# Optimization experiments

Hardware: AMD Instinct MI355X
Metric: run time of the kernel (lower is better)

## Reference

```python
import jax, jax.numpy as jnp
import numpy as np

HIDDEN = 1024
B, S = 4, 2048

def setup_inputs() -> dict:
    key = jax.random.key(0)
    k1, k2 = jax.random.split(key)
    qkv = jax.random.normal(k1, (B, S, HIDDEN), dtype=jnp.float32)
    mask = jnp.ones((B, S), dtype=jnp.float32)
    W_qkv = jax.random.normal(k2, (HIDDEN, 3 * HIDDEN), dtype=jnp.float32) * (HIDDEN ** -0.5)
    b_qkv = jnp.zeros((3 * HIDDEN,), dtype=jnp.float32)
    return {"qkv": qkv, "mask": mask, "W_qkv": W_qkv, "b_qkv": b_qkv}

def reference(qkv, mask, W_qkv, b_qkv):
    scale = HIDDEN ** -0.5
    proj = jnp.einsum("bsi,ih->bsh", qkv, W_qkv) + b_qkv  # [B,S,3H]
    q, k, v = jnp.split(proj, 3, axis=-1)                  # each [B,S,H]
    q = q * scale
    scores = jnp.einsum("bqh,bkh->bqk", q, k)              # [B,S,S]
    scores = scores + (1.0 - mask)[:, None, :] * -10000.0
    dist = jax.nn.softmax(scores, axis=-1)                 # dropout = identity (eval)
    return jnp.einsum("bqk,bkh->bqh", dist, v)             # [B,S,H]
```

## Files before the change

### kernel.cpp

```cpp
#include <hip/hip_runtime.h>
#include <hip/hip_bf16.h>

#define HID   1024
#define H3    3072
#define SEQ   2048
#define NB    4
#define MTOT  8192

typedef __bf16 bf16;
typedef bf16  bf16x4 __attribute__((ext_vector_type(4)));
typedef bf16  bf16x8 __attribute__((ext_vector_type(8)));
typedef float f32x4  __attribute__((ext_vector_type(4)));

#define MFMA16(a, b, c) __builtin_amdgcn_mfma_f32_16x16x32_bf16((a), (b), (c), 0, 0, 0)

#define GLOAD_LDS16(gp, lp)                                                     \
    __builtin_amdgcn_global_load_lds(                                           \
        (const __attribute__((address_space(1))) void*)(gp),                    \
        (__attribute__((address_space(3))) void*)(lp), 16, 0, 0)

#define FENCE() asm volatile("" ::: "memory")

__device__ __forceinline__ void stage_half(
    const bf16* __restrict__ G, long ld, long row0, long col0,
    char* dstbase, int w, int lane)
{
    const int r  = lane >> 2;
    const int c0 = ((lane & 3) * 8) ^ (((lane >> 5) & 1) << 4);
#pragma unroll
    for (int l = 0; l < 2; ++l) {
        const int sh = l * 8 + w;
        const bf16* src = G + (row0 + (long)((sh >> 1) * 16 + r)) * ld
                            + col0 + ((sh & 1) * 32 + c0);
        GLOAD_LDS16(src, dstbase + sh * 1024);
    }
}

__device__ __forceinline__ void gemm256_core(
    const bf16* __restrict__ A, long lda,
    const bf16* __restrict__ Bt, long ldb,
    long m0, long n0, int NT, char* lds, f32x4 (&acc)[8][4])
{
    const int tid = threadIdx.x, lane = tid & 63, w = tid >> 6;
    const int lr = lane & 15, lkg = lane >> 4;
    const int subA = (w >> 2) * 8;
    const int subB = (w & 3) * 4;
    const int inner = lr * 64 + (((lkg * 8) ^ ((lr >> 3) << 4)) << 1);

    char* A0b = lds;
    char* B0b = lds + 32768;
    char* A1b = lds + 65536;
    char* B1b = lds + 98304;

    stage_half(A,  lda, m0,        0, A0b,          w, lane);
    stage_half(A,  lda, m0 + 128,  0, A0b + 16384,  w, lane);
    stage_half(Bt, ldb, n0,        0, B0b,          w, lane);
    stage_half(Bt, ldb, n0 + 128,  0, B0b + 16384,  w, lane);
    stage_half(Bt, ldb, n0,       64, B1b,          w, lane);
    stage_half(Bt, ldb, n0 + 128, 64, B1b + 16384,  w, lane);
    asm volatile("s_waitcnt vmcnt(0)" ::: "memory");
    __builtin_amdgcn_s_barrier();
    FENCE();

    bf16x8 aR[4][2], bR[4][2];

    for (int t = 0; t < NT; ++t) {
        char* Ac = (t & 1) ? A1b : A0b;
        char* Bc = (t & 1) ? B1b : B0b;
        char* An = (t & 1) ? A0b : A1b;
        const long kA = (long)(t + 1) * 64;
        const long kB = (long)(t + 2) * 64;
        const bool doA = (t + 1 < NT), doB = (t + 2 < NT);

#pragma unroll
        for (int mf = 0; mf < 4; ++mf)
#pragma unroll
            for (int ks = 0; ks < 2; ++ks)
                aR[mf][ks] = *(const bf16x8*)(Ac + ((subA + mf) * 2 + ks) * 1024 + inner);
#pragma unroll
        for (int nf = 0; nf < 2; ++nf)
#pragma unroll
            for (int ks = 0; ks < 2; ++ks)
                bR[nf][ks] = *(const bf16x8*)(Bc + ((subB + nf) * 2 + ks) * 1024 + inner);
        if (doA) stage_half(A, lda, m0, kA, An, w, lane);
        __builtin_amdgcn_s_barrier();
        __builtin_amdgcn_s_setprio(1);
#pragma unroll
        for (int mf = 0; mf < 4; ++mf)
#pragma unroll
            for (int nf = 0; nf < 2; ++nf)
#pragma unroll
                for (int ks = 0; ks < 2; ++ks)
                    acc[mf][nf] = MFMA16(aR[mf][ks], bR[nf][ks], acc[mf][nf]);
        __builtin_amdgcn_s_setprio(0);
        __builtin_amdgcn_s_barrier();
        FENCE();

#pragma unroll
        for (int nf = 0; nf < 2; ++nf)
#pragma unroll
            for (int ks = 0; ks < 2; ++ks)
                bR[2 + nf][ks] = *(const bf16x8*)(Bc + ((subB + 2 + nf) * 2 + ks) * 1024 + inner);
        if (doA) stage_half(A, lda, m0 + 128, kA, An + 16384, w, lane);
        __builtin_amdgcn_s_barrier();
        __builtin_amdgcn_s_setprio(1);
#pragma unroll
        for (int mf = 0; mf < 4; ++mf)
#pragma unroll
            for (int nf = 0; nf < 2; ++nf)
#pragma unroll
                for (int ks = 0; ks < 2; ++ks)
                    acc[mf][2 + nf] = MFMA16(aR[mf][ks], bR[2 + nf][ks], acc[mf][2 + nf]);
        __builtin_amdgcn_s_setprio(0);
        __builtin_amdgcn_s_barrier();
        FENCE();

#pragma unroll
        for (int mf = 0; mf < 4; ++mf)
#pragma unroll
            for (int ks = 0; ks < 2; ++ks)
                aR[mf][ks] = *(const bf16x8*)(Ac + ((subA + 4 + mf) * 2 + ks) * 1024 + inner);
        if (doB) stage_half(Bt, ldb, n0, kB, Bc, w, lane);
        __builtin_amdgcn_s_barrier();
        __builtin_amdgcn_s_setprio(1);
#pragma unroll
        for (int mf = 0; mf < 4; ++mf)
#pragma unroll
            for (int nf = 0; nf < 2; ++nf)
#pragma unroll
                for (int ks = 0; ks < 2; ++ks)
                    acc[4 + mf][nf] = MFMA16(aR[mf][ks], bR[nf][ks], acc[4 + mf][nf]);
        __builtin_amdgcn_s_setprio(0);
        __builtin_amdgcn_s_barrier();
        FENCE();

        if (doB) {
            stage_half(Bt, ldb, n0 + 128, kB, Bc + 16384, w, lane);
            asm volatile("s_waitcnt vmcnt(4)" ::: "memory");
        } else {
            asm volatile("s_waitcnt vmcnt(0)" ::: "memory");
        }
        __builtin_amdgcn_s_barrier();
        __builtin_amdgcn_s_setprio(1);
#pragma unroll
        for (int mf = 0; mf < 4; ++mf)
#pragma unroll
            for (int nf = 0; nf < 2; ++nf)
#pragma unroll
                for (int ks = 0; ks < 2; ++ks)
                    acc[4 + mf][2 + nf] = MFMA16(aR[mf][ks], bR[2 + nf][ks], acc[4 + mf][2 + nf]);
        __builtin_amdgcn_s_setprio(0);
        __builtin_amdgcn_s_barrier();
        FENCE();
    }
}

__global__ __launch_bounds__(256) void conv_kernel(
    const float* __restrict__ X, const float* __restrict__ W,
    bf16* __restrict__ Xb, bf16* __restrict__ Wt)
{
    __shared__ bf16 T[64][66];
    const int bid = blockIdx.x;
    if (bid < 4096) {
        const long i = ((long)bid * 256 + threadIdx.x) * 8;
        float4 a = *(const float4*)(X + i);
        float4 b = *(const float4*)(X + i + 4);
        bf16x8 o;
        o[0] = (bf16)a.x; o[1] = (bf16)a.y; o[2] = (bf16)a.z; o[3] = (bf16)a.w;
        o[4] = (bf16)b.x; o[5] = (bf16)b.y; o[6] = (bf16)b.z; o[7] = (bf16)b.w;
        *(bf16x8*)(Xb + i) = o;
    } else {
        const int b2 = bid - 4096;
        const int n0 = (b2 % 48) * 64, k0 = (b2 / 48) * 64;
        const int r = threadIdx.x >> 2, s = threadIdx.x & 3;
        const float* wp = W + (size_t)(k0 + r) * H3 + n0 + s * 16;
#pragma unroll
        for (int q = 0; q < 4; ++q) {
            float4 a = *(const float4*)(wp + q * 4);
            T[r][s * 16 + q * 4 + 0] = (bf16)a.x;
            T[r][s * 16 + q * 4 + 1] = (bf16)a.y;
            T[r][s * 16 + q * 4 + 2] = (bf16)a.z;
            T[r][s * 16 + q * 4 + 3] = (bf16)a.w;
        }
        __syncthreads();
        bf16x8 o0, o1;
#pragma unroll
        for (int i = 0; i < 8; ++i) o0[i] = T[s * 16 + i][r];
#pragma unroll
        for (int i = 0; i < 8; ++i) o1[i] = T[s * 16 + 8 + i][r];
        bf16* op = Wt + (size_t)(n0 + r) * HID + k0 + s * 16;
        *(bf16x8*)op       = o0;
        *(bf16x8*)(op + 8) = o1;
    }
}

__global__ __launch_bounds__(512, 2) void proj_gemm2(
    const bf16* __restrict__ Xb, const bf16* __restrict__ Wt,
    const float* __restrict__ bias,
    bf16* __restrict__ Qb, bf16* __restrict__ Kb, bf16* __restrict__ Vt)
{
    __shared__ __attribute__((aligned(16))) char lds[135168];
    const int x = blockIdx.x & 7, q = blockIdx.x >> 3;
    const int bn = q >> 2, bm = x * 4 + (q & 3);

    f32x4 acc[8][4] = {};
    gemm256_core(Xb, HID, Wt, HID, (long)bm * 256, (long)bn * 256, 16, lds, acc);

    const int tid = threadIdx.x, lane = tid & 63, w = tid >> 6;
    const int lr = lane & 15, lkg = lane >> 4;
    const int wmL = (w >> 2) * 128;
    const int wnL = (w & 3) * 64;
    const int seg = bn >> 2;

    __syncthreads();
    bf16* sm_ = (bf16*)lds;

    if (seg < 2) {
        const float qs = (seg == 0) ? 0.03125f : 1.0f;
#pragma unroll
        for (int nf = 0; nf < 4; ++nf) {
            const int nl = wnL + nf * 16 + lr;
            const float bv = bias[bn * 256 + nl];
#pragma unroll
            for (int mf = 0; mf < 8; ++mf) {
                const int ml = wmL + mf * 16 + lkg * 4;
#pragma unroll
                for (int j = 0; j < 4; ++j)
                    sm_[(ml + j) * 264 + nl] = (bf16)((acc[mf][nf][j] + bv) * qs);
            }
        }
        __syncthreads();
        bf16* dst = (seg == 0) ? Qb : Kb;
        const long colbase = (long)(bn & 3) * 256;
        const long rowbase = (long)bm * 256;
#pragma unroll
        for (int it = 0; it < 16; ++it) {
            const int ml = (tid >> 5) + it * 16;
            const int nc = (tid & 31) * 8;
            bf16x8 vv = *(const bf16x8*)&sm_[ml * 264 + nc];
            *(bf16x8*)&dst[(rowbase + ml) * HID + colbase + nc] = vv;
        }
    } else {
#pragma unroll
        for (int nf = 0; nf < 4; ++nf) {
            const int nl = wnL + nf * 16 + lr;
            const float bv = bias[bn * 256 + nl];
#pragma unroll
            for (int mf = 0; mf < 8; ++mf) {
                const int ml = wmL + mf * 16 + lkg * 4;
                bf16x4 pk;
#pragma unroll
                for (int j = 0; j < 4; ++j) pk[j] = (bf16)(acc[mf][nf][j] + bv);
                *(bf16x4*)&sm_[nl * 264 + ml] = pk;
            }
        }
        __syncthreads();
        const int  bb = bm >> 3;
        const long s0 = (long)(bm & 7) * 256;
        const long h0 = (long)bn * 256 - 2048;
#pragma unroll
        for (int it = 0; it < 16; ++it) {
            const int nl = (tid >> 5) + it * 16;
            const int mc = (tid & 31) * 8;
            bf16x8 vv = *(const bf16x8*)&sm_[nl * 264 + mc];
            *(bf16x8*)&Vt[((long)(bb << 10) + h0 + nl) * SEQ + s0 + mc] = vv;
        }
    }
}

__global__ __launch_bounds__(512, 2) void qk_gemm2(
    const bf16* __restrict__ Qb, const bf16* __restrict__ Kb,
    float* __restrict__ Sc, int b_base)
{
    __shared__ __attribute__((aligned(16))) char lds[131072];
    const int z = blockIdx.z, b = b_base + z;

    f32x4 acc[8][4] = {};
    gemm256_core(Qb + (size_t)b * SEQ * HID, HID,
                 Kb + (size_t)b * SEQ * HID, HID,
                 (long)blockIdx.x * 256, (long)blockIdx.y * 256, 16, lds, acc);

    const int tid = threadIdx.x, lane = tid & 63, w = tid >> 6;
    const int lr = lane & 15, lkg = lane >> 4;
    const int m0i = (int)blockIdx.x * 256 + (w >> 2) * 128;
    const int n0i = (int)blockIdx.y * 256 + (w & 3) * 64;
    float* C = Sc + (size_t)z * SEQ * SEQ;
#pragma unroll
    for (int mf = 0; mf < 8; ++mf)
#pragma unroll
        for (int j = 0; j < 4; ++j) {
            const int row = m0i + mf * 16 + lkg * 4 + j;
#pragma unroll
            for (int nf = 0; nf < 4; ++nf)
                C[(size_t)row * SEQ + n0i + nf * 16 + lr] = acc[mf][nf][j];
        }
}

__device__ __forceinline__ void gemm128_core(
    const bf16* __restrict__ A, long lda,
    const bf16* __restrict__ Bt, long ldb,
    long m0, long n0, int ksteps,
    bf16* As, bf16* Bs, f32x4 acc[4][4])
{
    const int tid  = threadIdx.x;
    const int lane = tid & 63;
    const int w    = tid >> 6;
    const int lr   = lane & 15;
    const int lkg  = lane >> 4;
    const int wm   = (w >> 1) * 64, wn = (w & 1) * 64;

    const int srow   = w * 16 + (lane >> 2);
    const int schunk = (lane & 3) * 8;

    const bf16* ga0 = A  + (m0 + srow) * lda + schunk;
    const bf16* ga1 = ga0 + 64 * lda;
    const bf16* gb0 = Bt + (n0 + srow) * ldb + schunk;
    const bf16* gb1 = gb0 + 64 * ldb;
    bf16* lA = As + w * 512;
    bf16* lB = Bs + w * 512;

    for (int kt = 0; kt < ksteps; ++kt) {
        const long k0 = (long)kt * 32;
        __syncthreads();
        GLOAD_LDS16(ga0 + k0, lA);
        GLOAD_LDS16(ga1 + k0, lA + 2048);
        GLOAD_LDS16(gb0 + k0, lB);
        GLOAD_LDS16(gb1 + k0, lB + 2048);
        __syncthreads();

        bf16x8 af[4], bf_[4];
#pragma unroll
        for (int mi = 0; mi < 4; ++mi)
            af[mi] = *(const bf16x8*)&As[(wm + mi * 16 + lr) * 32 + lkg * 8];
#pragma unroll
        for (int ni = 0; ni < 4; ++ni)
            bf_[ni] = *(const bf16x8*)&Bs[(wn + ni * 16 + lr) * 32 + lkg * 8];
#pragma unroll
        for (int mi = 0; mi < 4; ++mi)
#pragma unroll
            for (int ni = 0; ni < 4; ++ni)
                acc[mi][ni] = MFMA16(af[mi], bf_[ni], acc[mi][ni]);
    }
}

__global__ __launch_bounds__(256) void sm_kernel(
    float* __restrict__ Sc, const float* __restrict__ mask, int b_base)
{
    __shared__ float redm[4], reds[4];
    const long row = blockIdx.x;
    const int  z = (int)(row >> 11);
    const int  b = b_base + z;
    const int tid = threadIdx.x, lane = tid & 63, w = tid >> 6;

    float* sp = Sc + row * SEQ;
    float v[8];
    {
        float4 a = *(const float4*)(sp + tid * 8);
        float4 c = *(const float4*)(sp + tid * 8 + 4);
        const float* mp = mask + (size_t)b * SEQ + tid * 8;
        float4 m0 = *(const float4*)mp;
        float4 m1 = *(const float4*)(mp + 4);
        v[0] = a.x + (1.0f - m0.x) * -10000.0f;
        v[1] = a.y + (1.0f - m0.y) * -10000.0f;
        v[2] = a.z + (1.0f - m0.z) * -10000.0f;
        v[3] = a.w + (1.0f - m0.w) * -10000.0f;
        v[4] = c.x + (1.0f - m1.x) * -10000.0f;
        v[5] = c.y + (1.0f - m1.y) * -10000.0f;
        v[6] = c.z + (1.0f - m1.z) * -10000.0f;
        v[7] = c.w + (1.0f - m1.w) * -10000.0f;
    }
    float mx = v[0];
#pragma unroll
    for (int i = 1; i < 8; ++i) mx = fmaxf(mx, v[i]);
#pragma unroll
    for (int d = 1; d < 64; d <<= 1) mx = fmaxf(mx, __shfl_xor(mx, d));
    if (lane == 0) redm[w] = mx;
    __syncthreads();
    mx = fmaxf(fmaxf(redm[0], redm[1]), fmaxf(redm[2], redm[3]));

    float s = 0.0f;
#pragma unroll
    for (int i = 0; i < 8; ++i) { v[i] = __expf(v[i] - mx); s += v[i]; }
#pragma unroll
    for (int d = 1; d < 64; d <<= 1) s += __shfl_xor(s, d);
    if (lane == 0) reds[w] = s;
    __syncthreads();
    s = reds[0] + reds[1] + reds[2] + reds[3];
    const float inv = 1.0f / s;

    bf16x8 o;
#pragma unroll
    for (int i = 0; i < 8; ++i) o[i] = (bf16)(v[i] * inv);
    *(bf16x8*)((bf16*)sp + tid * 8) = o;
}

__global__ __launch_bounds__(256) void pv_gemm(
    const bf16* __restrict__ P, const bf16* __restrict__ Vt,
    float* __restrict__ out, int b_base)
{
    __shared__ bf16 As[128 * 32], Bs[128 * 32];
    const int z = blockIdx.z, b = b_base + z;
    const bf16* A  = P  + (size_t)z * SEQ * 4096;
    const bf16* Bt = Vt + (size_t)b * HID * SEQ;
    f32x4 acc[4][4] = {};
    gemm128_core(A, 4096, Bt, SEQ, (long)blockIdx.x * 128, (long)blockIdx.y * 128,
                 64, As, Bs, acc);

    const int tid = threadIdx.x, lane = tid & 63, w = tid >> 6;
    const int lr = lane & 15, lkg = lane >> 4;
    const int wm = (w >> 1) * 64, wn = (w & 1) * 64;
    float* C = out + (size_t)b * SEQ * HID;
#pragma unroll
    for (int mi = 0; mi < 4; ++mi)
#pragma unroll
        for (int j = 0; j < 4; ++j) {
            const int row = (int)blockIdx.x * 128 + wm + mi * 16 + lkg * 4 + j;
#pragma unroll
            for (int ni = 0; ni < 4; ++ni) {
                const int col = (int)blockIdx.y * 128 + wn + ni * 16 + lr;
                C[(size_t)row * HID + col] = acc[mi][ni][j];
            }
        }
}

extern "C" void kernel_launch(void* const* d_in, const int* in_sizes, int n_in,
                              void* d_out, int out_size, void* d_ws, size_t ws_size,
                              hipStream_t stream)
{
    const float* X    = (const float*)d_in[0];
    const float* mask = (const float*)d_in[1];
    const float* W    = (const float*)d_in[2];
    const float* bias = (const float*)d_in[3];
    float* out = (float*)d_out;

    char* ws = (char*)d_ws;
    const size_t MB = 1024 * 1024;
    bf16* Qb = (bf16*)ws;
    bf16* Kb = (bf16*)(ws + 16 * MB);
    bf16* Vt = (bf16*)(ws + 32 * MB);
    bf16*  Xb = (bf16*)(ws + 48 * MB);
    bf16*  Wt = (bf16*)(ws + 64 * MB);
    float* Sc = (float*)(ws + 48 * MB);

    int nbg;
    if      (ws_size >= 112 * MB) nbg = 4;
    else if (ws_size >=  80 * MB) nbg = 2;
    else                          nbg = 1;

    conv_kernel<<<4096 + 768, 256, 0, stream>>>(X, W, Xb, Wt);
    proj_gemm2<<<384, 512, 0, stream>>>(Xb, Wt, bias, Qb, Kb, Vt);

    for (int g = 0; g < NB / nbg; ++g) {
        const int b0 = g * nbg;
        qk_gemm2<<<dim3(8, 8, nbg), 512, 0, stream>>>(Qb, Kb, Sc, b0);
        sm_kernel<<<nbg * SEQ, 256, 0, stream>>>(Sc, mask, b0);
        pv_gemm<<<dim3(16, 8, nbg), 256, 0, stream>>>((const bf16*)Sc, Vt, out, b0);
    }
}
```

Measured before the change: 188.0 us.

## Replace PV GEMM with pipelined 128x256 tile kernel using swizzled LDS double buffering

The PV GEMM moves from a simple 128x128 tile kernel with 256 threads and synchronous global-to-LDS loads per 32-wide k step to a 512-thread, 128x256 tile kernel. The new core stages 64-wide k slices into double-buffered, XOR-swizzled LDS with asynchronous global_load_lds prefetch one or two steps ahead, and interleaves MFMA quadrants with barriers and priority hints. The aim is to hide load latency, raise reuse per tile and avoid LDS bank conflicts. It uses 96KB of LDS per block and halves the grid in the N dimension, which lowers occupancy and parallelism.

```diff
diff --git a/kernel.cpp b/kernel.cpp
--- a/kernel.cpp
+++ b/kernel.cpp
@@ -149,6 +149,125 @@
 #pragma unroll
                 for (int ks = 0; ks < 2; ++ks)
                     acc[4 + mf][2 + nf] = MFMA16(aR[mf][ks], bR[2 + nf][ks], acc[4 + mf][2 + nf]);
+        __builtin_amdgcn_s_setprio(0);
+        __builtin_amdgcn_s_barrier();
+        FENCE();
+    }
+}
+
+__device__ __forceinline__ void gemm_h_core(
+    const bf16* __restrict__ A, long lda,
+    const bf16* __restrict__ Bt, long ldb,
+    long m0, long n0, int NT, char* lds, f32x4 (&acc)[4][4])
+{
+    const int tid = threadIdx.x, lane = tid & 63, w = tid >> 6;
+    const int lr = lane & 15, lkg = lane >> 4;
+    const int subA = (w >> 2) * 4;
+    const int subB = (w & 3) * 4;
+    const int inner = lr * 64 + (((lkg * 8) ^ ((lr >> 3) << 4)) << 1);
+
+    char* A0b = lds;
+    char* B0b = lds + 16384;
+    char* A1b = lds + 49152;
+    char* B1b = lds + 65536;
+
+    stage_half(A,  lda, m0,        0, A0b,          w, lane);
+    stage_half(Bt, ldb, n0,        0, B0b,          w, lane);
+    stage_half(Bt, ldb, n0 + 128,  0, B0b + 16384,  w, lane);
+    stage_half(Bt, ldb, n0,       64, B1b,          w, lane);
+    stage_half(Bt, ldb, n0 + 128, 64, B1b + 16384,  w, lane);
+    asm volatile("s_waitcnt vmcnt(0)" ::: "memory");
+    __builtin_amdgcn_s_barrier();
+    FENCE();
+
+    bf16x8 aR[2][2], bR[4][2];
+
+    for (int t = 0; t < NT; ++t) {
+        char* Ac = (t & 1) ? A1b : A0b;
+        char* Bc = (t & 1) ? B1b : B0b;
+        char* An = (t & 1) ? A0b : A1b;
+        const long kA = (long)(t + 1) * 64;
+        const long kB = (long)(t + 2) * 64;
+        const bool doA = (t + 1 < NT), doB = (t + 2 < NT);
+
+#pragma unroll
+        for (int mf = 0; mf < 2; ++mf)
+#pragma unroll
+            for (int ks = 0; ks < 2; ++ks)
+                aR[mf][ks] = *(const bf16x8*)(Ac + ((subA + mf) * 2 + ks) * 1024 + inner);
+#pragma unroll
+        for (int nf = 0; nf < 2; ++nf)
+#pragma unroll
+            for (int ks = 0; ks < 2; ++ks)
+                bR[nf][ks] = *(const bf16x8*)(Bc + ((subB + nf) * 2 + ks) * 1024 + inner);
+        if (doA) stage_half(A, lda, m0, kA, An, w, lane);
+        __builtin_amdgcn_s_barrier();
+        __builtin_amdgcn_s_setprio(1);
+#pragma unroll
+        for (int mf = 0; mf < 2; ++mf)
+#pragma unroll
+            for (int nf = 0; nf < 2; ++nf)
+#pragma unroll
+                for (int ks = 0; ks < 2; ++ks)
+                    acc[mf][nf] = MFMA16(aR[mf][ks], bR[nf][ks], acc[mf][nf]);
+        __builtin_amdgcn_s_setprio(0);
+        __builtin_amdgcn_s_barrier();
+        FENCE();
+
+#pragma unroll
+        for (int nf = 0; nf < 2; ++nf)
+#pragma unroll
+            for (int ks = 0; ks < 2; ++ks)
+                bR[2 + nf][ks] = *(const bf16x8*)(Bc + ((subB + 2 + nf) * 2 + ks) * 1024 + inner);
+        __builtin_amdgcn_s_barrier();
+        __builtin_amdgcn_s_setprio(1);
+#pragma unroll
+        for (int mf = 0; mf < 2; ++mf)
+#pragma unroll
+            for (int nf = 0; nf < 2; ++nf)
+#pragma unroll
+                for (int ks = 0; ks < 2; ++ks)
+                    acc[mf][2 + nf] = MFMA16(aR[mf][ks], bR[2 + nf][ks], acc[mf][2 + nf]);
+        __builtin_amdgcn_s_setprio(0);
+        __builtin_amdgcn_s_barrier();
+        FENCE();
+
+#pragma unroll
+        for (int mf = 0; mf < 2; ++mf)
+#pragma unroll
+            for (int ks = 0; ks < 2; ++ks)
+                aR[mf][ks] = *(const bf16x8*)(Ac + ((subA + 2 + mf) * 2 + ks) * 1024 + inner);
+        if (doB) {
+            stage_half(Bt, ldb, n0,       kB, Bc,         w, lane);
+            stage_half(Bt, ldb, n0 + 128, kB, Bc + 16384, w, lane);
+        }
+        __builtin_amdgcn_s_barrier();
+        __builtin_amdgcn_s_setprio(1);
+#pragma unroll
+        for (int mf = 0; mf < 2; ++mf)
+#pragma unroll
+            for (int nf = 0; nf < 2; ++nf)
+#pragma unroll
+                for (int ks = 0; ks < 2; ++ks)
+                    acc[2 + mf][nf] = MFMA16(aR[mf][ks], bR[nf][ks], acc[2 + mf][nf]);
+        __builtin_amdgcn_s_setprio(0);
+        __builtin_amdgcn_s_barrier();
+        FENCE();
+
+        if (doB) {
+            asm volatile("s_waitcnt vmcnt(4)" ::: "memory");
+        } else {
+            asm volatile("s_waitcnt vmcnt(0)" ::: "memory");
+        }
+        __builtin_amdgcn_s_barrier();
+        __builtin_amdgcn_s_setprio(1);
+#pragma unroll
+        for (int mf = 0; mf < 2; ++mf)
+#pragma unroll
+            for (int nf = 0; nf < 2; ++nf)
+#pragma unroll
+                for (int ks = 0; ks < 2; ++ks)
+                    acc[2 + mf][2 + nf] = MFMA16(aR[mf][ks], bR[2 + nf][ks], acc[2 + mf][2 + nf]);
         __builtin_amdgcn_s_setprio(0);
         __builtin_amdgcn_s_barrier();
         FENCE();
@@ -294,53 +413,6 @@
             for (int nf = 0; nf < 4; ++nf)
                 C[(size_t)row * SEQ + n0i + nf * 16 + lr] = acc[mf][nf][j];
         }
-}
-
-__device__ __forceinline__ void gemm128_core(
-    const bf16* __restrict__ A, long lda,
-    const bf16* __restrict__ Bt, long ldb,
-    long m0, long n0, int ksteps,
-    bf16* As, bf16* Bs, f32x4 acc[4][4])
-{
-    const int tid  = threadIdx.x;
-    const int lane = tid & 63;
-    const int w    = tid >> 6;
-    const int lr   = lane & 15;
-    const int lkg  = lane >> 4;
-    const int wm   = (w >> 1) * 64, wn = (w & 1) * 64;
-
-    const int srow   = w * 16 + (lane >> 2);
-    const int schunk = (lane & 3) * 8;
-
-    const bf16* ga0 = A  + (m0 + srow) * lda + schunk;
-    const bf16* ga1 = ga0 + 64 * lda;
-    const bf16* gb0 = Bt + (n0 + srow) * ldb + schunk;
-    const bf16* gb1 = gb0 + 64 * ldb;
-    bf16* lA = As + w * 512;
-    bf16* lB = Bs + w * 512;
-
-    for (int kt = 0; kt < ksteps; ++kt) {
-        const long k0 = (long)kt * 32;
-        __syncthreads();
-        GLOAD_LDS16(ga0 + k0, lA);
-        GLOAD_LDS16(ga1 + k0, lA + 2048);
-        GLOAD_LDS16(gb0 + k0, lB);
-        GLOAD_LDS16(gb1 + k0, lB + 2048);
-        __syncthreads();
-
-        bf16x8 af[4], bf_[4];
-#pragma unroll
-        for (int mi = 0; mi < 4; ++mi)
-            af[mi] = *(const bf16x8*)&As[(wm + mi * 16 + lr) * 32 + lkg * 8];
-#pragma unroll
-        for (int ni = 0; ni < 4; ++ni)
-            bf_[ni] = *(const bf16x8*)&Bs[(wn + ni * 16 + lr) * 32 + lkg * 8];
-#pragma unroll
-        for (int mi = 0; mi < 4; ++mi)
-#pragma unroll
-            for (int ni = 0; ni < 4; ++ni)
-                acc[mi][ni] = MFMA16(af[mi], bf_[ni], acc[mi][ni]);
-    }
 }
 
 __global__ __launch_bounds__(256) void sm_kernel(
@@ -394,32 +466,31 @@
     *(bf16x8*)((bf16*)sp + tid * 8) = o;
 }
 
-__global__ __launch_bounds__(256) void pv_gemm(
+__global__ __launch_bounds__(512, 2) void pv_gemm2(
     const bf16* __restrict__ P, const bf16* __restrict__ Vt,
     float* __restrict__ out, int b_base)
 {
-    __shared__ bf16 As[128 * 32], Bs[128 * 32];
+    __shared__ __attribute__((aligned(16))) char lds[98304];
     const int z = blockIdx.z, b = b_base + z;
-    const bf16* A  = P  + (size_t)z * SEQ * 4096;
-    const bf16* Bt = Vt + (size_t)b * HID * SEQ;
+
     f32x4 acc[4][4] = {};
-    gemm128_core(A, 4096, Bt, SEQ, (long)blockIdx.x * 128, (long)blockIdx.y * 128,
-                 64, As, Bs, acc);
+    gemm_h_core(P + (size_t)z * SEQ * 4096, 4096,
+                Vt + (size_t)b * HID * SEQ, SEQ,
+                (long)blockIdx.x * 128, (long)blockIdx.y * 256, 32, lds, acc);
 
     const int tid = threadIdx.x, lane = tid & 63, w = tid >> 6;
     const int lr = lane & 15, lkg = lane >> 4;
-    const int wm = (w >> 1) * 64, wn = (w & 1) * 64;
+    const int m0i = (int)blockIdx.x * 128 + (w >> 2) * 64;
+    const int n0i = (int)blockIdx.y * 256 + (w & 3) * 64;
     float* C = out + (size_t)b * SEQ * HID;
 #pragma unroll
-    for (int mi = 0; mi < 4; ++mi)
+    for (int mf = 0; mf < 4; ++mf)
 #pragma unroll
         for (int j = 0; j < 4; ++j) {
-            const int row = (int)blockIdx.x * 128 + wm + mi * 16 + lkg * 4 + j;
-#pragma unroll
-            for (int ni = 0; ni < 4; ++ni) {
-                const int col = (int)blockIdx.y * 128 + wn + ni * 16 + lr;
-                C[(size_t)row * HID + col] = acc[mi][ni][j];
-            }
+            const int row = m0i + mf * 16 + lkg * 4 + j;
+#pragma unroll
+            for (int nf = 0; nf < 4; ++nf)
+                C[(size_t)row * HID + n0i + nf * 16 + lr] = acc[mf][nf][j];
         }
 }
 
@@ -454,6 +525,6 @@
         const int b0 = g * nbg;
         qk_gemm2<<<dim3(8, 8, nbg), 512, 0, stream>>>(Qb, Kb, Sc, b0);
         sm_kernel<<<nbg * SEQ, 256, 0, stream>>>(Sc, mask, b0);
-        pv_gemm<<<dim3(16, 8, nbg), 256, 0, stream>>>((const bf16*)Sc, Vt, out, b0);
-    }
-}
+        pv_gemm2<<<dim3(16, 4, nbg), 512, 0, stream>>>((const bf16*)Sc, Vt, out, b0);
+    }
+}
```

After: 172.4 us. 1.09x faster.
